# Optimization experiments

Measured on AMD Instinct MI355X. Metric: run time of the kernel, lower is better.

## Reference

```python
import jax, jax.numpy as jnp
import numpy as np

DT = 0.001
TAU_MEM = 0.02
TAU_SYN = 0.005
THRESHOLD = 1.0


def conv2d(x, w, b, stride, pad):
    # x: [N,C,H,W], w: [O,I,kh,kw]
    y = jax.lax.conv_general_dilated(
        x, w, window_strides=(stride, stride),
        padding=[(pad, pad), (pad, pad)],
        dimension_numbers=("NCHW", "OIHW", "NCHW"))
    return y + b[None, :, None, None]


def lif_scan(current_t_first):
    # current_t_first: [T, B, C, H, W]; LIF with reset='subtract'
    alpha = jnp.exp(jnp.asarray(-DT / TAU_MEM, dtype=current_t_first.dtype))
    beta = jnp.exp(jnp.asarray(-DT / TAU_SYN, dtype=current_t_first.dtype))
    state_shape = current_t_first.shape[1:]
    init = (jnp.zeros(state_shape, current_t_first.dtype),
            jnp.zeros(state_shape, current_t_first.dtype))

    def step(carry, i_t):
        syn, mem = carry
        syn = beta * syn + i_t
        mem = alpha * mem + syn
        spike = (mem >= THRESHOLD).astype(i_t.dtype)
        mem = mem - THRESHOLD * spike  # subtract reset
        return (syn, mem), spike

    _, spikes = jax.lax.scan(step, init, current_t_first)
    return spikes  # [T, B, C, H, W]


def spiking_conv(x, w, b, stride, pad):
    # x: [B, C, H, W, T] -> spikes [B, O, H', W', T]
    B, C, H, W, T = x.shape
    xt = jnp.moveaxis(x, -1, 0)                 # [T,B,C,H,W]
    y = conv2d(xt.reshape(T * B, C, H, W), w, b, stride, pad)
    y = y.reshape(T, B, *y.shape[1:])           # [T,B,O,H',W']
    spikes = lif_scan(y)
    return jnp.moveaxis(spikes, 0, -1)          # [B,O,H',W',T]


def setup_inputs() -> dict:
    key = jax.random.key(0)
    ks = jax.random.split(key, 9)
    B, H, W, T = 4, 128, 128, 10
    num_classes = 80
    det_ch = (num_classes + 5) * 3  # 255

    def init_w(k, shape):
        fan_in = shape[1] * shape[2] * shape[3]
        bound = 1.0 / np.sqrt(fan_in)
        return jax.random.uniform(k, shape, jnp.float32, -bound, bound)

    x = jax.random.uniform(ks[0], (B, 2, H, W, T), jnp.float32)
    return {
        "x": x,
        "w1": init_w(ks[1], (64, 2, 3, 3)),   "b1": jax.random.uniform(ks[2], (64,), jnp.float32, -0.2, 0.2),
        "w2": init_w(ks[3], (128, 64, 3, 3)), "b2": jax.random.uniform(ks[4], (128,), jnp.float32, -0.04, 0.04),
        "w3": init_w(ks[5], (256, 128, 3, 3)),"b3": jax.random.uniform(ks[6], (256,), jnp.float32, -0.03, 0.03),
        "wd": init_w(ks[7], (det_ch, 256, 1, 1)), "bd": jax.random.uniform(ks[8], (det_ch,), jnp.float32, -0.06, 0.06),
    }


def reference(x, w1, b1, w2, b2, w3, b3, wd, bd):
    h = spiking_conv(x, w1, b1, stride=1, pad=1)   # [B,64,128,128,T]
    h = spiking_conv(h, w2, b2, stride=2, pad=1)   # [B,128,64,64,T]
    h = spiking_conv(h, w3, b3, stride=2, pad=1)   # [B,256,32,32,T]
    h_pooled = jnp.mean(h, axis=-1)                # mean over time
    detections = conv2d(h_pooled, wd, bd, stride=1, pad=0)  # [B,255,32,32]
    return detections
```

## Files before the change

### kernel.cpp

```cpp
#include <hip/hip_runtime.h>
#include <stdint.h>
#include <string.h>
#include <cmath>


#define BB 4
#define TT 10

typedef short bf16x8 __attribute__((ext_vector_type(8)));
typedef float f32x4  __attribute__((ext_vector_type(4)));

#define MFMA16(a, b, c) __builtin_amdgcn_mfma_f32_16x16x32_bf16((a), (b), (c), 0, 0, 0)


__global__ __launch_bounds__(256) void zpad1v(uint32_t* __restrict__ buf) {
    uint32_t* p = buf + (size_t)blockIdx.x * 544896u;
    for (int i = threadIdx.x; i < 8320; i += 256) {
        if (i < 4224) p[i] = 0u;
        else {
            int j = i - 4224;
            int row = 1 + (j >> 5), cih = (j >> 4) & 1, e = j & 15;
            p[row * 4224 + 2112 + cih * 1056 + e] = 0u;
        }
    }
}

__global__ __launch_bounds__(256) void zpad3v(uint32_t* __restrict__ buf) {
    uint32_t* p = buf + (size_t)blockIdx.x * 282880u;
    for (int i = threadIdx.x; i < 8448; i += 256) {
        if (i < 4352) p[i] = 0u;
        else {
            int j = i - 4352;
            int row = 1 + (j >> 6), cih = (j >> 4) & 3, e = j & 15;
            p[row * 4352 + 2176 + cih * 544 + e] = 0u;
        }
    }
}

__global__ __launch_bounds__(256) void conv1_lif(
    const float* __restrict__ x,
    const float* __restrict__ w1,
    const float* __restrict__ b1,
    unsigned short* __restrict__ s1p2,
    float alpha, float beta)
{
    __shared__ float xs[2][3][10][10];
    __shared__ float wsh[18][64];
    __shared__ uint32_t spk[40][68];
    const int tid = threadIdx.x;
    const int b = blockIdx.z, h = blockIdx.y, w0 = blockIdx.x * 8;

    for (int i = tid; i < 1152; i += 256) {
        int co = i & 63, tap = i >> 6;
        wsh[tap][co] = w1[co * 18 + tap];
    }
    for (int i = tid; i < 600; i += 256) {
        int t = i % 10; int rest = i / 10;
        int wi = rest % 10; rest /= 10;
        int kh = rest % 3; int ci = rest / 3;
        int hh = h - 1 + kh, ww = w0 - 1 + wi;
        float v = 0.f;
        if (hh >= 0 && hh < 128 && ww >= 0 && ww < 128)
            v = x[(((b * 2 + ci) * 128 + hh) * 128 + ww) * 10 + t];
        xs[ci][kh][wi][t] = v;
    }
    __syncthreads();

    const int px  = tid & 7;
    const int cog = (tid >> 3) * 2;
    float acc[2][10];
#pragma unroll
    for (int c = 0; c < 2; ++c)
#pragma unroll
        for (int t = 0; t < 10; ++t) acc[c][t] = 0.f;

#pragma unroll
    for (int tap = 0; tap < 18; ++tap) {
        const int ci = tap / 9, kh = (tap % 9) / 3, kw = tap % 3;
        float2 wv = *(const float2*)&wsh[tap][cog];
#pragma unroll
        for (int t = 0; t < 10; ++t) {
            float xv = xs[ci][kh][px + kw][t];
            acc[0][t] = __fmaf_rn(wv.x, xv, acc[0][t]);
            acc[1][t] = __fmaf_rn(wv.y, xv, acc[1][t]);
        }
    }
    const int pr    = px & 1;
    const int col2l = px >> 1;
    const int comb0 = pr * 2 + (cog >> 5);
    const int ipos  = col2l * 16 + ((cog & 31) >> 1);
    const float bv0 = b1[cog], bv1 = b1[cog + 1];
    float syn0 = 0.f, mem0 = 0.f, syn1 = 0.f, mem1 = 0.f;
#pragma unroll
    for (int t = 0; t < 10; ++t) {
        float cur0 = __fadd_rn(acc[0][t], bv0);
        syn0 = __fadd_rn(__fmul_rn(beta, syn0), cur0);
        mem0 = __fadd_rn(__fmul_rn(alpha, mem0), syn0);
        bool s0 = (mem0 >= 1.0f);
        mem0 = __fsub_rn(mem0, s0 ? 1.0f : 0.0f);
        float cur1 = __fadd_rn(acc[1][t], bv1);
        syn1 = __fadd_rn(__fmul_rn(beta, syn1), cur1);
        mem1 = __fadd_rn(__fmul_rn(alpha, mem1), syn1);
        bool s1 = (mem1 >= 1.0f);
        mem1 = __fsub_rn(mem1, s1 ? 1.0f : 0.0f);
        spk[t * 4 + comb0][ipos] =
            (s0 ? 0x3F80u : 0u) | ((s1 ? 0x3F80u : 0u) << 16);
    }
    __syncthreads();

    uint32_t* sg = (uint32_t*)s1p2;
    const int e = tid & 63;
#pragma unroll
    for (int k = 0; k < 10; ++k) {
        const int combo = k * 4 + (tid >> 6);
        const int t  = combo >> 2;
        const int pp = (combo >> 1) & 1;
        const int ch = combo & 1;
        const uint32_t ga = (uint32_t)(t * BB + b) * 544896u
            + ((uint32_t)((h + 1) * 8448 + pp * 4224 + ch * 2112
                          + ((w0 >> 1) + pp) * 32) >> 1) + e;
        sg[ga] = spk[combo][e];
    }
}

__global__ __launch_bounds__(256) void wtrans2c(
    const float* __restrict__ w2, unsigned short* __restrict__ wtb)
{
    int i = blockIdx.x * 256 + threadIdx.x;
    if (i >= 73728) return;
    int co  = i / 576;
    int rem = i - co * 576;
    int ci  = rem / 9;
    int tap = rem - ci * 9;
    float w = w2[i];
    uint32_t uw  = __float_as_uint(w);
    uint32_t h16 = (uw + 0x7FFFu + ((uw >> 16) & 1u)) >> 16;
    float hf = __uint_as_float(h16 << 16);
    float r1 = w - hf;
    uint32_t ur1 = __float_as_uint(r1);
    uint32_t m16 = (ur1 + 0x7FFFu + ((ur1 >> 16) & 1u)) >> 16;
    float mf = __uint_as_float(m16 << 16);
    float r2 = r1 - mf;
    uint32_t ur2 = __float_as_uint(r2);
    uint32_t l16 = (ur2 + 0x7FFFu + ((ur2 >> 16) & 1u)) >> 16;

    int cobi = co >> 6, coL = co & 63;
    int wid = coL >> 4, l15 = coL & 15;
    int c = ci >> 5, r5 = ci & 31;
    int g = r5 >> 3, e = r5 & 7;
    size_t base = (size_t)(cobi * 27 + tap * 3) * 4096
                + (size_t)(((wid * 2 + c) * 64 + (g * 16 + l15)) * 8 + e);
    wtb[base]        = (unsigned short)h16;
    wtb[base + 4096] = (unsigned short)m16;
    wtb[base + 8192] = (unsigned short)l16;
}

__global__ __launch_bounds__(256) void wtrans3c(
    const float* __restrict__ w3, unsigned short* __restrict__ wtb)
{
    int i = blockIdx.x * 256 + threadIdx.x;
    if (i >= 294912) return;
    int co  = i / 1152;
    int rem = i - co * 1152;
    int ci  = rem / 9;
    int tap = rem - ci * 9;
    float w = w3[i];
    uint32_t uw  = __float_as_uint(w);
    uint32_t h16 = (uw + 0x7FFFu + ((uw >> 16) & 1u)) >> 16;
    float hf = __uint_as_float(h16 << 16);
    float r1 = w - hf;
    uint32_t ur1 = __float_as_uint(r1);
    uint32_t m16 = (ur1 + 0x7FFFu + ((ur1 >> 16) & 1u)) >> 16;
    float mf = __uint_as_float(m16 << 16);
    float r2 = r1 - mf;
    uint32_t ur2 = __float_as_uint(r2);
    uint32_t l16 = (ur2 + 0x7FFFu + ((ur2 >> 16) & 1u)) >> 16;

    int cobi = co >> 6, coL = co & 63;
    int wq = coL >> 4, l15 = coL & 15;
    int cc = ci >> 5, r5 = ci & 31;
    int g = r5 >> 3, e = r5 & 7;
    size_t base = (size_t)(cobi * 27 + tap * 3) * 8192
                + (size_t)(((wq * 4 + cc) * 64 + (g * 16 + l15)) * 8 + e);
    wtb[base]         = (unsigned short)h16;
    wtb[base + 8192]  = (unsigned short)m16;
    wtb[base + 16384] = (unsigned short)l16;
}

#define VMCNT(n) do { __builtin_amdgcn_sched_barrier(0); \
    asm volatile("s_waitcnt vmcnt(" #n ")" ::: "memory"); \
    __builtin_amdgcn_sched_barrier(0); } while (0)
#define SB() __builtin_amdgcn_sched_barrier(0)
#define BARR() do { __builtin_amdgcn_sched_barrier(0); \
    __builtin_amdgcn_s_barrier(); \
    __builtin_amdgcn_sched_barrier(0); } while (0)
#define PRIO1() __builtin_amdgcn_s_setprio(1)
#define PRIO0() __builtin_amdgcn_s_setprio(0)

__global__ __launch_bounds__(256) void conv2_mfma(
    const unsigned short* __restrict__ s1p2,
    const unsigned short* __restrict__ wtb,
    float* __restrict__ p2)
{
    __shared__ alignas(16) unsigned short Bs[3][4096];
    const int tid  = threadIdx.x;
    const int lane = tid & 63, w = tid >> 6;
    const int r = lane & 15, g = lane >> 4;
    const int f = blockIdx.z;
    const int cobi = blockIdx.y;
    const int hb = blockIdx.x;

    const unsigned short* fb = s1p2 + (uint32_t)f * 1089792u;
    const unsigned short* wB = wtb + (uint32_t)cobi * (27u * 4096u)
                             + (uint32_t)w * 1024u + (uint32_t)lane * 8u;
    const uint32_t lfo = (uint32_t)(r * 32 + g * 8);

    f32x4 acc[4];
#pragma unroll
    for (int mt = 0; mt < 4; ++mt) acc[mt] = (f32x4){0.f, 0.f, 0.f, 0.f};
    bf16x8 bA[6], bB[6];

#define STAGE2(tap_, slot_) do { \
    const int kh_ = (tap_) / 3, kw_ = (tap_) % 3; \
    const int p_ = (kw_ == 1) ? 0 : 1; \
    const int cf_ = (kw_ == 2) ? 1 : 0; \
    _Pragma("unroll") \
    for (int c_ = 0; c_ < 2; ++c_) { \
        const unsigned short* src_ = fb + (uint32_t)(2 * hb + kh_) * 8448u \
            + (uint32_t)p_ * 4224u + (uint32_t)c_ * 2112u \
            + (uint32_t)(w * 16 + cf_) * 32u + lfo; \
        __builtin_amdgcn_global_load_lds( \
            (const __attribute__((address_space(1))) unsigned int*)(const void*)src_, \
            (__attribute__((address_space(3))) unsigned int*)(void*)(&Bs[slot_][(w * 2 + c_) * 512]), \
            16, 0, 0); \
    } } while (0)

#define LOADB2(tap_, DST) do { _Pragma("unroll") \
    for (int t_ = 0; t_ < 3; ++t_) { _Pragma("unroll") \
        for (int c_ = 0; c_ < 2; ++c_) \
            DST[t_ * 2 + c_] = *(const bf16x8*)(wB + (uint32_t)((tap_) * 3 + t_) * 4096u + c_ * 512u); \
    } } while (0)

#define COMP2(slot_, BU) do { \
    bf16x8 af_[8]; \
    _Pragma("unroll") \
    for (int q_ = 0; q_ < 8; ++q_) \
        af_[q_] = *(const bf16x8*)&Bs[slot_][q_ * 512 + lane * 8]; \
    _Pragma("unroll") \
    for (int t_ = 0; t_ < 3; ++t_) { _Pragma("unroll") \
        for (int c_ = 0; c_ < 2; ++c_) { \
            bf16x8 b_ = BU[t_ * 2 + c_]; \
            acc[0] = MFMA16(b_, af_[0 + c_], acc[0]); \
            acc[1] = MFMA16(b_, af_[2 + c_], acc[1]); \
            acc[2] = MFMA16(b_, af_[4 + c_], acc[2]); \
            acc[3] = MFMA16(b_, af_[6 + c_], acc[3]); \
        } } } while (0)

#define PH2(tap_, snxt_, scur_, BU, BN) do { \
    SB(); STAGE2((tap_) + 1, snxt_); LOADB2((tap_) + 1, BN); SB(); \
    VMCNT(8); BARR(); \
    PRIO1(); COMP2(scur_, BU); PRIO0(); SB(); \
} while (0)

    STAGE2(0, 0); LOADB2(0, bA);
    PH2(0, 1, 0, bA, bB); PH2(1, 2, 1, bB, bA); PH2(2, 0, 2, bA, bB);
    PH2(3, 1, 0, bB, bA); PH2(4, 2, 1, bA, bB); PH2(5, 0, 2, bB, bA);
    PH2(6, 1, 0, bA, bB); PH2(7, 2, 1, bB, bA);
    SB(); VMCNT(0); BARR();
    PRIO1(); COMP2(2, bA); PRIO0();

#pragma unroll
    for (int mt = 0; mt < 4; ++mt)
        *(f32x4*)&p2[((uint32_t)f * 4096u + hb * 64 + mt * 16 + r) * 128u
                     + cobi * 64 + w * 16 + g * 4] = acc[mt];
#undef STAGE2
#undef LOADB2
#undef COMP2
#undef PH2
}

__global__ __launch_bounds__(256) void lif_s2_t(
    const float* __restrict__ pa, const float* __restrict__ bias,
    unsigned short* __restrict__ s2p3, float alpha, float beta)
{
    const int tid = threadIdx.x;
    const int b   = blockIdx.z;
    const int px  = blockIdx.x * 8 + (tid >> 5);
    const int co0 = (tid & 31) * 4;
    const int h = px >> 6, w = px & 63;
    float4 bv = *(const float4*)&bias[co0];
    const float bva[4] = {bv.x, bv.y, bv.z, bv.w};
    float syn[4] = {0.f,0.f,0.f,0.f}, mem[4] = {0.f,0.f,0.f,0.f};
    const int pr = w & 1;
    const int col2 = (w + pr) >> 1;
    unsigned short* sp = s2p3 + (uint32_t)(h + 1) * 8704u + pr * 4352u
                       + (co0 >> 5) * 1088u + col2 * 32u + (co0 & 31);
    for (int t = 0; t < TT; ++t) {
        const int f = t * BB + b;
        const uint32_t idx = ((uint32_t)f * 4096u + px) * 128u + co0;
        float4 A = *(const float4*)&pa[idx];
        const float va[4] = {A.x, A.y, A.z, A.w};
        uint32_t pk[2] = {0u, 0u};
#pragma unroll
        for (int j = 0; j < 4; ++j) {
            float c = __fadd_rn(va[j], bva[j]);
            syn[j] = __fadd_rn(__fmul_rn(beta, syn[j]), c);
            mem[j] = __fadd_rn(__fmul_rn(alpha, mem[j]), syn[j]);
            bool sc = (mem[j] >= 1.0f);
            mem[j] = __fsub_rn(mem[j], sc ? 1.0f : 0.0f);
            pk[j >> 1] |= (sc ? 0x3F80u : 0u) << ((j & 1) * 16);
        }
        *(uint2*)(sp + (uint32_t)f * 565760u) = make_uint2(pk[0], pk[1]);
    }
}

__global__ __launch_bounds__(256) void conv3_mfma3(
    const unsigned short* __restrict__ s2p3,
    const unsigned short* __restrict__ wtb,
    float* __restrict__ p3)
{
    __shared__ alignas(16) unsigned short Bs[3][4096];
    const int tid  = threadIdx.x;
    const int lane = tid & 63, w = tid >> 6;
    const int r = lane & 15, g = lane >> 4;
    const int f = blockIdx.z;
    const int cobi = blockIdx.y;
    const int h0 = blockIdx.x * 2;

    const unsigned short* fb = s2p3 + (uint32_t)f * 565760u;
    const unsigned short* wB = wtb + (uint32_t)cobi * (27u * 8192u)
                             + (uint32_t)w * 2048u + (uint32_t)lane * 8u;
    const uint32_t lfo = (uint32_t)(r * 32 + g * 8);

    f32x4 acc[4];
#pragma unroll
    for (int mt = 0; mt < 4; ++mt) acc[mt] = (f32x4){0.f, 0.f, 0.f, 0.f};
    bf16x8 bA[6], bB[6];

#define STAGE3(tap_, half_, slot_) do { \
    const int kh_ = (tap_) / 3, kw_ = (tap_) % 3; \
    const int p_ = (kw_ == 1) ? 0 : 1; \
    const int cf_ = (kw_ == 2) ? 1 : 0; \
    _Pragma("unroll") \
    for (int j_ = 0; j_ < 2; ++j_) { \
        const unsigned short* src_ = fb \
            + (uint32_t)(2 * (h0 + (w >> 1)) + kh_) * 8704u \
            + (uint32_t)p_ * 4352u + (uint32_t)((half_) * 2 + j_) * 1088u \
            + (uint32_t)((w & 1) * 16 + cf_) * 32u + lfo; \
        __builtin_amdgcn_global_load_lds( \
            (const __attribute__((address_space(1))) unsigned int*)(const void*)src_, \
            (__attribute__((address_space(3))) unsigned int*)(void*)(&Bs[slot_][(w * 2 + j_) * 512]), \
            16, 0, 0); \
    } } while (0)

#define LOADB3(tap_, half_, DST) do { _Pragma("unroll") \
    for (int t_ = 0; t_ < 3; ++t_) { _Pragma("unroll") \
        for (int j_ = 0; j_ < 2; ++j_) \
            DST[t_ * 2 + j_] = *(const bf16x8*)(wB + (uint32_t)((tap_) * 3 + t_) * 8192u \
                + (uint32_t)((half_) * 2 + j_) * 512u); \
    } } while (0)

#define COMP3(slot_, BU) do { \
    bf16x8 af_[8]; \
    _Pragma("unroll") \
    for (int q_ = 0; q_ < 8; ++q_) \
        af_[q_] = *(const bf16x8*)&Bs[slot_][q_ * 512 + lane * 8]; \
    _Pragma("unroll") \
    for (int t_ = 0; t_ < 3; ++t_) { _Pragma("unroll") \
        for (int j_ = 0; j_ < 2; ++j_) { \
            bf16x8 b_ = BU[t_ * 2 + j_]; \
            acc[0] = MFMA16(af_[0 + j_], b_, acc[0]); \
            acc[1] = MFMA16(af_[2 + j_], b_, acc[1]); \
            acc[2] = MFMA16(af_[4 + j_], b_, acc[2]); \
            acc[3] = MFMA16(af_[6 + j_], b_, acc[3]); \
        } } } while (0)

#define PH3(ntap_, nhalf_, snxt_, scur_, BU, BN) do { \
    SB(); STAGE3(ntap_, nhalf_, snxt_); LOADB3(ntap_, nhalf_, BN); SB(); \
    VMCNT(8); BARR(); \
    PRIO1(); COMP3(scur_, BU); PRIO0(); SB(); \
} while (0)

    STAGE3(0, 0, 0); LOADB3(0, 0, bA);
    PH3(0, 1, 1, 0, bA, bB); PH3(1, 0, 2, 1, bB, bA); PH3(1, 1, 0, 2, bA, bB);
    PH3(2, 0, 1, 0, bB, bA); PH3(2, 1, 2, 1, bA, bB); PH3(3, 0, 0, 2, bB, bA);
    PH3(3, 1, 1, 0, bA, bB); PH3(4, 0, 2, 1, bB, bA); PH3(4, 1, 0, 2, bA, bB);
    PH3(5, 0, 1, 0, bB, bA); PH3(5, 1, 2, 1, bA, bB); PH3(6, 0, 0, 2, bB, bA);
    PH3(6, 1, 1, 0, bA, bB); PH3(7, 0, 2, 1, bB, bA); PH3(7, 1, 0, 2, bA, bB);
    PH3(8, 0, 1, 0, bB, bA); PH3(8, 1, 2, 1, bA, bB);
    SB(); VMCNT(0); BARR();
    PRIO1(); COMP3(2, bB); PRIO0();

#pragma unroll
    for (int mt = 0; mt < 4; ++mt) {
        const int hh = h0 + (mt >> 1);
        const int wc = (mt & 1) * 16 + g * 4;
        *(f32x4*)&p3[((uint32_t)(f * 256 + cobi * 64 + w * 16 + r) * 32u + hh) * 32u + wc] = acc[mt];
    }
#undef STAGE3
#undef LOADB3
#undef COMP3
#undef PH3
}

__global__ __launch_bounds__(256) void lif_mean1(
    const float* __restrict__ p3, const float* __restrict__ bias,
    float* __restrict__ pooled, float alpha, float beta)
{
    const int px = (blockIdx.x * 256 + threadIdx.x) * 4;
    const int co = blockIdx.y;
    const int b  = blockIdx.z;
    const float bv = bias[co];
    float syn[4] = {0.f,0.f,0.f,0.f}, mem[4] = {0.f,0.f,0.f,0.f};
    float sum[4] = {0.f,0.f,0.f,0.f};
    for (int t = 0; t < TT; ++t) {
        const int idx = ((t * BB + b) * 256 + co) * 1024 + px;
        float4 a = *(const float4*)&p3[idx];
        const float va[4] = {a.x, a.y, a.z, a.w};
#pragma unroll
        for (int j = 0; j < 4; ++j) {
            float cu = __fadd_rn(va[j], bv);
            syn[j] = __fadd_rn(__fmul_rn(beta, syn[j]), cu);
            mem[j] = __fadd_rn(__fmul_rn(alpha, mem[j]), syn[j]);
            bool sc = (mem[j] >= 1.0f);
            float sp = sc ? 1.0f : 0.0f;
            mem[j] = __fsub_rn(mem[j], sp);
            sum[j] = __fadd_rn(sum[j], sp);
        }
    }
    *(float4*)&pooled[(b * 256 + co) * 1024 + px] =
        make_float4(sum[0] / 10.0f, sum[1] / 10.0f, sum[2] / 10.0f, sum[3] / 10.0f);
}

__global__ __launch_bounds__(256) void det_conv(
    const float* __restrict__ pooled,
    const float* __restrict__ wd,
    const float* __restrict__ bd,
    float* __restrict__ out)
{
    __shared__ float wtl[16][64];
    __shared__ float ps[16][64];
    const int tid = threadIdx.x;
    const int b = blockIdx.z;
    const int o_base = blockIdx.y * 64;
    const int px_base = blockIdx.x * 64;
    const int o_off = (tid >> 4) * 4;
    const int px_off = (tid & 15) * 4;
    float acc[4][4];
#pragma unroll
    for (int c = 0; c < 4; ++c) {
        int o = o_base + o_off + c;
        float bv = (o < 255) ? bd[o] : 0.f;
#pragma unroll
        for (int j = 0; j < 4; ++j) acc[c][j] = bv;
    }
    for (int cc = 0; cc < 16; ++cc) {
        for (int k = tid; k < 1024; k += 256) {
            int o = k & 63, ci = k >> 6;
            wtl[ci][o] = (o_base + o < 255) ? wd[(o_base + o) * 256 + cc * 16 + ci] : 0.f;
            ps[ci][o] = pooled[(b * 256 + cc * 16 + ci) * 1024 + px_base + o];
        }
        __syncthreads();
#pragma unroll
        for (int ci = 0; ci < 16; ++ci) {
            float4 wv = *(const float4*)&wtl[ci][o_off];
            float4 sv = *(const float4*)&ps[ci][px_off];
            acc[0][0] += wv.x * sv.x; acc[0][1] += wv.x * sv.y;
            acc[0][2] += wv.x * sv.z; acc[0][3] += wv.x * sv.w;
            acc[1][0] += wv.y * sv.x; acc[1][1] += wv.y * sv.y;
            acc[1][2] += wv.y * sv.z; acc[1][3] += wv.y * sv.w;
            acc[2][0] += wv.z * sv.x; acc[2][1] += wv.z * sv.y;
            acc[2][2] += wv.z * sv.z; acc[2][3] += wv.z * sv.w;
            acc[3][0] += wv.w * sv.x; acc[3][1] += wv.w * sv.y;
            acc[3][2] += wv.w * sv.z; acc[3][3] += wv.w * sv.w;
        }
        __syncthreads();
    }
#pragma unroll
    for (int c = 0; c < 4; ++c) {
        int o = o_base + o_off + c;
        if (o < 255)
            *(float4*)&out[(b * 255 + o) * 1024 + px_base + px_off] =
                make_float4(acc[c][0], acc[c][1], acc[c][2], acc[c][3]);
    }
}

extern "C" void kernel_launch(void* const* d_in, const int* in_sizes, int n_in,
                              void* d_out, int out_size, void* d_ws, size_t ws_size,
                              hipStream_t stream) {
    const float* x  = (const float*)d_in[0];
    const float* w1 = (const float*)d_in[1];
    const float* b1 = (const float*)d_in[2];
    const float* w2 = (const float*)d_in[3];
    const float* b2 = (const float*)d_in[4];
    const float* w3 = (const float*)d_in[5];
    const float* b3 = (const float*)d_in[6];
    const float* wd = (const float*)d_in[7];
    const float* bd = (const float*)d_in[8];
    float* out = (float*)d_out;

    uint8_t* wsb = (uint8_t*)d_ws;
    unsigned short* s1p2 = (unsigned short*)(wsb + 256);
    float*   p3     = (float*)(wsb + 256);
    float*   p2     = (float*)(wsb + 87183616u);
    float*   pooled = (float*)(wsb + 87183616u);
    unsigned short* s2p3 = (unsigned short*)(wsb + 171069696u);
    unsigned short* wt2b = (unsigned short*)(wsb + 216330496u);
    unsigned short* wt3b = (unsigned short*)(wsb + 216772864u);

    float alpha, beta;
    { uint32_t ab = 0x3F7383C6u; memcpy(&alpha, &ab, 4); }
    { uint32_t bb = 0x3F519857u; memcpy(&beta,  &bb, 4); }

    zpad1v<<<40, 256, 0, stream>>>((uint32_t*)s1p2);
    zpad3v<<<40, 256, 0, stream>>>((uint32_t*)s2p3);
    wtrans2c<<<288, 256, 0, stream>>>(w2, wt2b);
    wtrans3c<<<1152, 256, 0, stream>>>(w3, wt3b);
    conv1_lif<<<dim3(16, 128, 4), 256, 0, stream>>>(x, w1, b1, s1p2, alpha, beta);
    conv2_mfma<<<dim3(64, 2, 40), 256, 0, stream>>>(s1p2, wt2b, p2);
    lif_s2_t<<<dim3(512, 1, 4), 256, 0, stream>>>(p2, b2, s2p3, alpha, beta);
    conv3_mfma3<<<dim3(16, 4, 40), 256, 0, stream>>>(s2p3, wt3b, p3);
    lif_mean1<<<dim3(1, 256, 4), 256, 0, stream>>>(p3, b3, pooled, alpha, beta);
    det_conv<<<dim3(16, 4, 4), 256, 0, stream>>>(pooled, wd, bd, out);
}
```

Before: 310.3 us.

## Load conv activation fragments directly to registers instead of staging through LDS

Conv2 and conv3 MFMA kernels drop the shared-memory triple buffer filled by global_load_lds. Each wave now loads its activation fragments from global memory straight into double-buffered registers, which removes LDS traffic and the per-tap block barriers. In exchange every wave loads the full activation tile itself, so global/L2 traffic rises about fourfold. The added register buffers also raise register pressure, which may cut occupancy.

```diff
diff --git a/kernel.cpp b/kernel.cpp
--- a/kernel.cpp
+++ b/kernel.cpp
@@ -191,9 +191,6 @@
     asm volatile("s_waitcnt vmcnt(" #n ")" ::: "memory"); \
     __builtin_amdgcn_sched_barrier(0); } while (0)
 #define SB() __builtin_amdgcn_sched_barrier(0)
-#define BARR() do { __builtin_amdgcn_sched_barrier(0); \
-    __builtin_amdgcn_s_barrier(); \
-    __builtin_amdgcn_sched_barrier(0); } while (0)
 #define PRIO1() __builtin_amdgcn_s_setprio(1)
 #define PRIO0() __builtin_amdgcn_s_setprio(0)
 
@@ -202,7 +199,6 @@
     const unsigned short* __restrict__ wtb,
     float* __restrict__ p2)
 {
-    __shared__ alignas(16) unsigned short Bs[3][4096];
     const int tid  = threadIdx.x;
     const int lane = tid & 63, w = tid >> 6;
     const int r = lane & 15, g = lane >> 4;
@@ -218,21 +214,18 @@
     f32x4 acc[4];
 #pragma unroll
     for (int mt = 0; mt < 4; ++mt) acc[mt] = (f32x4){0.f, 0.f, 0.f, 0.f};
-    bf16x8 bA[6], bB[6];
-
-#define STAGE2(tap_, slot_) do { \
+    bf16x8 aA[8], aB[8], bA[6], bB[6];
+
+#define LOADA2(tap_, DST) do { \
     const int kh_ = (tap_) / 3, kw_ = (tap_) % 3; \
     const int p_ = (kw_ == 1) ? 0 : 1; \
     const int cf_ = (kw_ == 2) ? 1 : 0; \
     _Pragma("unroll") \
-    for (int c_ = 0; c_ < 2; ++c_) { \
-        const unsigned short* src_ = fb + (uint32_t)(2 * hb + kh_) * 8448u \
+    for (int q_ = 0; q_ < 8; ++q_) { \
+        const int mt_ = q_ >> 1, c_ = q_ & 1; \
+        DST[q_] = *(const bf16x8*)(fb + (uint32_t)(2 * hb + kh_) * 8448u \
             + (uint32_t)p_ * 4224u + (uint32_t)c_ * 2112u \
-            + (uint32_t)(w * 16 + cf_) * 32u + lfo; \
-        __builtin_amdgcn_global_load_lds( \
-            (const __attribute__((address_space(1))) unsigned int*)(const void*)src_, \
-            (__attribute__((address_space(3))) unsigned int*)(void*)(&Bs[slot_][(w * 2 + c_) * 512]), \
-            16, 0, 0); \
+            + (uint32_t)(mt_ * 16 + cf_) * 32u + lfo); \
     } } while (0)
 
 #define LOADB2(tap_, DST) do { _Pragma("unroll") \
@@ -241,39 +234,35 @@
             DST[t_ * 2 + c_] = *(const bf16x8*)(wB + (uint32_t)((tap_) * 3 + t_) * 4096u + c_ * 512u); \
     } } while (0)
 
-#define COMP2(slot_, BU) do { \
-    bf16x8 af_[8]; \
-    _Pragma("unroll") \
-    for (int q_ = 0; q_ < 8; ++q_) \
-        af_[q_] = *(const bf16x8*)&Bs[slot_][q_ * 512 + lane * 8]; \
-    _Pragma("unroll") \
+#define COMP2(AU, BU) do { _Pragma("unroll") \
     for (int t_ = 0; t_ < 3; ++t_) { _Pragma("unroll") \
         for (int c_ = 0; c_ < 2; ++c_) { \
             bf16x8 b_ = BU[t_ * 2 + c_]; \
-            acc[0] = MFMA16(b_, af_[0 + c_], acc[0]); \
-            acc[1] = MFMA16(b_, af_[2 + c_], acc[1]); \
-            acc[2] = MFMA16(b_, af_[4 + c_], acc[2]); \
-            acc[3] = MFMA16(b_, af_[6 + c_], acc[3]); \
+            acc[0] = MFMA16(b_, AU[0 + c_], acc[0]); \
+            acc[1] = MFMA16(b_, AU[2 + c_], acc[1]); \
+            acc[2] = MFMA16(b_, AU[4 + c_], acc[2]); \
+            acc[3] = MFMA16(b_, AU[6 + c_], acc[3]); \
         } } } while (0)
 
-#define PH2(tap_, snxt_, scur_, BU, BN) do { \
-    SB(); STAGE2((tap_) + 1, snxt_); LOADB2((tap_) + 1, BN); SB(); \
-    VMCNT(8); BARR(); \
-    PRIO1(); COMP2(scur_, BU); PRIO0(); SB(); \
+#define PH2(tap_, AU, BU, AN, BN) do { \
+    SB(); LOADA2((tap_) + 1, AN); LOADB2((tap_) + 1, BN); SB(); \
+    VMCNT(14); \
+    PRIO1(); COMP2(AU, BU); PRIO0(); SB(); \
 } while (0)
 
-    STAGE2(0, 0); LOADB2(0, bA);
-    PH2(0, 1, 0, bA, bB); PH2(1, 2, 1, bB, bA); PH2(2, 0, 2, bA, bB);
-    PH2(3, 1, 0, bB, bA); PH2(4, 2, 1, bA, bB); PH2(5, 0, 2, bB, bA);
-    PH2(6, 1, 0, bA, bB); PH2(7, 2, 1, bB, bA);
-    SB(); VMCNT(0); BARR();
-    PRIO1(); COMP2(2, bA); PRIO0();
+    LOADA2(0, aA); LOADB2(0, bA);
+    PH2(0, aA, bA, aB, bB); PH2(1, aB, bB, aA, bA);
+    PH2(2, aA, bA, aB, bB); PH2(3, aB, bB, aA, bA);
+    PH2(4, aA, bA, aB, bB); PH2(5, aB, bB, aA, bA);
+    PH2(6, aA, bA, aB, bB); PH2(7, aB, bB, aA, bA);
+    SB(); VMCNT(0);
+    PRIO1(); COMP2(aA, bA); PRIO0();
 
 #pragma unroll
     for (int mt = 0; mt < 4; ++mt)
         *(f32x4*)&p2[((uint32_t)f * 4096u + hb * 64 + mt * 16 + r) * 128u
                      + cobi * 64 + w * 16 + g * 4] = acc[mt];
-#undef STAGE2
+#undef LOADA2
 #undef LOADB2
 #undef COMP2
 #undef PH2
@@ -319,7 +308,6 @@
     const unsigned short* __restrict__ wtb,
     float* __restrict__ p3)
 {
-    __shared__ alignas(16) unsigned short Bs[3][4096];
     const int tid  = threadIdx.x;
     const int lane = tid & 63, w = tid >> 6;
     const int r = lane & 15, g = lane >> 4;
@@ -335,22 +323,19 @@
     f32x4 acc[4];
 #pragma unroll
     for (int mt = 0; mt < 4; ++mt) acc[mt] = (f32x4){0.f, 0.f, 0.f, 0.f};
-    bf16x8 bA[6], bB[6];
-
-#define STAGE3(tap_, half_, slot_) do { \
+    bf16x8 aA[8], aB[8], bA[6], bB[6];
+
+#define LOADA3(tap_, half_, DST) do { \
     const int kh_ = (tap_) / 3, kw_ = (tap_) % 3; \
     const int p_ = (kw_ == 1) ? 0 : 1; \
     const int cf_ = (kw_ == 2) ? 1 : 0; \
     _Pragma("unroll") \
-    for (int j_ = 0; j_ < 2; ++j_) { \
-        const unsigned short* src_ = fb \
-            + (uint32_t)(2 * (h0 + (w >> 1)) + kh_) * 8704u \
+    for (int q_ = 0; q_ < 8; ++q_) { \
+        const int mt_ = q_ >> 1, j_ = q_ & 1; \
+        DST[q_] = *(const bf16x8*)(fb \
+            + (uint32_t)(2 * (h0 + (mt_ >> 1)) + kh_) * 8704u \
             + (uint32_t)p_ * 4352u + (uint32_t)((half_) * 2 + j_) * 1088u \
-            + (uint32_t)((w & 1) * 16 + cf_) * 32u + lfo; \
-        __builtin_amdgcn_global_load_lds( \
-            (const __attribute__((address_space(1))) unsigned int*)(const void*)src_, \
-            (__attribute__((address_space(3))) unsigned int*)(void*)(&Bs[slot_][(w * 2 + j_) * 512]), \
-            16, 0, 0); \
+            + (uint32_t)((mt_ & 1) * 16 + cf_) * 32u + lfo); \
     } } while (0)
 
 #define LOADB3(tap_, half_, DST) do { _Pragma("unroll") \
@@ -360,36 +345,34 @@
                 + (uint32_t)((half_) * 2 + j_) * 512u); \
     } } while (0)
 
-#define COMP3(slot_, BU) do { \
-    bf16x8 af_[8]; \
-    _Pragma("unroll") \
-    for (int q_ = 0; q_ < 8; ++q_) \
-        af_[q_] = *(const bf16x8*)&Bs[slot_][q_ * 512 + lane * 8]; \
-    _Pragma("unroll") \
+#define COMP3(AU, BU) do { _Pragma("unroll") \
     for (int t_ = 0; t_ < 3; ++t_) { _Pragma("unroll") \
         for (int j_ = 0; j_ < 2; ++j_) { \
             bf16x8 b_ = BU[t_ * 2 + j_]; \
-            acc[0] = MFMA16(af_[0 + j_], b_, acc[0]); \
-            acc[1] = MFMA16(af_[2 + j_], b_, acc[1]); \
-            acc[2] = MFMA16(af_[4 + j_], b_, acc[2]); \
-            acc[3] = MFMA16(af_[6 + j_], b_, acc[3]); \
+            acc[0] = MFMA16(AU[0 + j_], b_, acc[0]); \
+            acc[1] = MFMA16(AU[2 + j_], b_, acc[1]); \
+            acc[2] = MFMA16(AU[4 + j_], b_, acc[2]); \
+            acc[3] = MFMA16(AU[6 + j_], b_, acc[3]); \
         } } } while (0)
 
-#define PH3(ntap_, nhalf_, snxt_, scur_, BU, BN) do { \
-    SB(); STAGE3(ntap_, nhalf_, snxt_); LOADB3(ntap_, nhalf_, BN); SB(); \
-    VMCNT(8); BARR(); \
-    PRIO1(); COMP3(scur_, BU); PRIO0(); SB(); \
+#define PH3(ntap_, nhalf_, AU, BU, AN, BN) do { \
+    SB(); LOADA3(ntap_, nhalf_, AN); LOADB3(ntap_, nhalf_, BN); SB(); \
+    VMCNT(14); \
+    PRIO1(); COMP3(AU, BU); PRIO0(); SB(); \
 } while (0)
 
-    STAGE3(0, 0, 0); LOADB3(0, 0, bA);
-    PH3(0, 1, 1, 0, bA, bB); PH3(1, 0, 2, 1, bB, bA); PH3(1, 1, 0, 2, bA, bB);
-    PH3(2, 0, 1, 0, bB, bA); PH3(2, 1, 2, 1, bA, bB); PH3(3, 0, 0, 2, bB, bA);
-    PH3(3, 1, 1, 0, bA, bB); PH3(4, 0, 2, 1, bB, bA); PH3(4, 1, 0, 2, bA, bB);
-    PH3(5, 0, 1, 0, bB, bA); PH3(5, 1, 2, 1, bA, bB); PH3(6, 0, 0, 2, bB, bA);
-    PH3(6, 1, 1, 0, bA, bB); PH3(7, 0, 2, 1, bB, bA); PH3(7, 1, 0, 2, bA, bB);
-    PH3(8, 0, 1, 0, bB, bA); PH3(8, 1, 2, 1, bA, bB);
-    SB(); VMCNT(0); BARR();
-    PRIO1(); COMP3(2, bB); PRIO0();
+    LOADA3(0, 0, aA); LOADB3(0, 0, bA);
+    PH3(0, 1, aA, bA, aB, bB); PH3(1, 0, aB, bB, aA, bA);
+    PH3(1, 1, aA, bA, aB, bB); PH3(2, 0, aB, bB, aA, bA);
+    PH3(2, 1, aA, bA, aB, bB); PH3(3, 0, aB, bB, aA, bA);
+    PH3(3, 1, aA, bA, aB, bB); PH3(4, 0, aB, bB, aA, bA);
+    PH3(4, 1, aA, bA, aB, bB); PH3(5, 0, aB, bB, aA, bA);
+    PH3(5, 1, aA, bA, aB, bB); PH3(6, 0, aB, bB, aA, bA);
+    PH3(6, 1, aA, bA, aB, bB); PH3(7, 0, aB, bB, aA, bA);
+    PH3(7, 1, aA, bA, aB, bB); PH3(8, 0, aB, bB, aA, bA);
+    PH3(8, 1, aA, bA, aB, bB);
+    SB(); VMCNT(0);
+    PRIO1(); COMP3(aB, bB); PRIO0();
 
 #pragma unroll
     for (int mt = 0; mt < 4; ++mt) {
@@ -397,7 +380,7 @@
         const int wc = (mt & 1) * 16 + g * 4;
         *(f32x4*)&p3[((uint32_t)(f * 256 + cobi * 64 + w * 16 + r) * 32u + hh) * 32u + wc] = acc[mt];
     }
-#undef STAGE3
+#undef LOADA3
 #undef LOADB3
 #undef COMP3
 #undef PH3
```

Result: slower. 412.9 us (+33.1%).
